# Performance work log

Measured on AMD Instinct MI355X. Metric: run time of the kernel, lower is better.

The kernel has to match this reference:

```python
import jax, jax.numpy as jnp
import numpy as np

RBF_DIM = 64          # args.radius_emb_dim
FOLD_DIM = 128        # args.fold_dim
PROT_RADIUS = 30.0    # args.protein_radius (GaussianSmearing stop)
NP_, NL_, E_ = 100000, 50000, 500000


def gaussian_smearing(d):
    # GaussianSmearing(start=0, stop=PROT_RADIUS, num_gaussians=RBF_DIM)
    offsets = jnp.linspace(0.0, PROT_RADIUS, RBF_DIM, dtype=d.dtype)  # [R]
    coeff = -0.5 / (offsets[1] - offsets[0]) ** 2
    return jnp.exp(coeff * (d[:, None] - offsets[None, :]) ** 2)  # [E, R]


def setup_inputs() -> dict:
    key = jax.random.key(0)
    ks = jax.random.split(key, 12)
    scale = 10.0  # spread positions so distances span [0, PROT_RADIUS]
    pos = lambda k, n: jax.random.normal(k, (n, 3), jnp.float32) * scale
    inp = {
        'lig_pos': pos(ks[0], NL_),
        'prot_pos': pos(ks[1], NP_),
        'prot_pos_Cb': pos(ks[2], NP_),
        'prot_pos_C': pos(ks[3], NP_),
        'prot_pos_O': pos(ks[4], NP_),
        'prot_pos_N': pos(ks[5], NP_),
        'W1': jax.random.normal(ks[6], (5 * RBF_DIM, FOLD_DIM), jnp.float32) * 0.05,
        'b1': jnp.zeros((FOLD_DIM,), jnp.float32),
        'W2': jax.random.normal(ks[7], (FOLD_DIM, FOLD_DIM), jnp.float32) * 0.05,
        'b2': jnp.zeros((FOLD_DIM,), jnp.float32),
        'src': jax.random.randint(ks[8], (E_,), 0, NL_, jnp.int32),   # ligand index per edge
        'dst': jax.random.randint(ks[9], (E_,), 0, NP_, jnp.int32),   # protein index per edge
    }
    return inp


def reference(lig_pos, prot_pos, prot_pos_Cb, prot_pos_C, prot_pos_O, prot_pos_N,
              W1, b1, W2, b2, src, dst):
    lp = lig_pos[src]  # [E, 3] gather of ligand positions
    # 5 distance channels: CA/Cb/C/O/N protein atoms, each RBF-smeared
    feats = [gaussian_smearing(jnp.linalg.norm(lp - p[dst], axis=-1))
             for p in (prot_pos, prot_pos_Cb, prot_pos_C, prot_pos_O, prot_pos_N)]
    edge_attr = jnp.concatenate(feats, axis=-1)  # [E, 5*RBF_DIM]
    h = jax.nn.relu(edge_attr @ W1 + b1)         # [E, FOLD_DIM]
    return h @ W2 + b2                           # [E, FOLD_DIM]
```

## Files before the change

kernel.cpp:

```cpp
#include <hip/hip_runtime.h>
#include <hip/hip_bf16.h>

typedef unsigned short ushort_t;
typedef unsigned int uint_t;
typedef __attribute__((ext_vector_type(8))) short short8;
typedef __attribute__((ext_vector_type(4))) float f32x4;
typedef __attribute__((ext_vector_type(2))) uint_t uint2_t;

#define FOLD 128
#define S_CONST 1.78357580f
#define DS_CONST 0.84932180f

__device__ __forceinline__ uint_t pkbf(float a, float b) {
    __hip_bfloat162 h2 = __float22bfloat162_rn(float2{a, b});
    uint_t u;
    __builtin_memcpy(&u, &h2, sizeof(u));
    return u;
}

#define NWAVES 8
#define W1_OFF 0
#define W2_OFF 20480
#define B1_OFF 28672
#define B2_OFF 28800
#define H_OFF  28928
#define LDS_DW 37120

__global__ __launch_bounds__(512) void fused(
    const float* __restrict__ lig,
    const float* __restrict__ p0, const float* __restrict__ p1,
    const float* __restrict__ p2, const float* __restrict__ p3,
    const float* __restrict__ p4,
    const float* __restrict__ W1, const float* __restrict__ W2,
    const float* __restrict__ b1, const float* __restrict__ b2,
    const int* __restrict__ src, const int* __restrict__ dst,
    float* __restrict__ out, int E)
{
    extern __shared__ uint_t smem[];
    uint_t* W1L = smem + W1_OFF;
    uint_t* W2L = smem + W2_OFF;
    const float* b1L = (const float*)(smem + B1_OFF);
    const float* b2L = (const float*)(smem + B2_OFF);

    const int t = threadIdx.x;
    const int w = t >> 6;
    const int l = t & 63;
    const int eL = l & 15, g = l >> 4;
    uint_t* hw = smem + H_OFF + (w << 10);

    for (int idx = t; idx < 20480; idx += 512) {
        int jj = idx & 3, l2 = (idx >> 2) & 63, nt = (idx >> 8) & 7, ks = idx >> 11;
        int row = ks * 32 + ((l2 >> 4) << 3) + 2 * jj;
        int col = nt * 16 + (l2 & 15);
        W1L[idx] = pkbf(W1[row * FOLD + col], W1[(row + 1) * FOLD + col]);
    }
    for (int idx = t; idx < 8192; idx += 512) {
        int jj = idx & 3, l2 = (idx >> 2) & 63, nt = (idx >> 8) & 7, ks = idx >> 11;
        int row = ks * 32 + ((l2 >> 4) << 3) + 2 * jj;
        int col = nt * 16 + (l2 & 15);
        W2L[idx] = pkbf(W2[row * FOLD + col], W2[(row + 1) * FOLD + col]);
    }
    if (t < 128) ((float*)(smem + B1_OFF))[t] = b1[t];
    else if (t < 256) ((float*)(smem + B2_OFF))[t - 128] = b2[t - 128];
    __syncthreads();

    const int NT = (E + 31) >> 5;
    const int stride = gridDim.x * NWAVES;
    int wt = blockIdx.x * NWAVES + w;
    if (wt >= NT) return;

    const float* GP = (g == 0) ? p0 : (g == 1) ? p1 : (g == 2) ? p2 : p3;
    const bool g0 = (g == 0);
    const float gbase = (float)(8 * g) * DS_CONST;

    float Ax[2], Ay[2], Az[2], Px[2], Py[2], Pz[2], Qx[2], Qy[2], Qz[2];
    {
        #pragma unroll
        for (int eh = 0; eh < 2; ++eh) {
            int e = wt * 32 + eh * 16 + eL; if (e >= E) e = E - 1;
            int s = src[e], d2 = dst[e];
            Ax[eh] = lig[3 * s]; Ay[eh] = lig[3 * s + 1]; Az[eh] = lig[3 * s + 2];
            Px[eh] = GP[3 * d2]; Py[eh] = GP[3 * d2 + 1]; Pz[eh] = GP[3 * d2 + 2];
            if (g0) { Qx[eh] = p4[3 * d2]; Qy[eh] = p4[3 * d2 + 1]; Qz[eh] = p4[3 * d2 + 2]; }
        }
    }

    while (true) {
        const int wt2 = wt + stride;
        const bool more = (wt2 < NT);

        int sB[2], dB[2];
        if (more) {
            #pragma unroll
            for (int eh = 0; eh < 2; ++eh) {
                int e = wt2 * 32 + eh * 16 + eL; if (e >= E) e = E - 1;
                sB[eh] = src[e]; dB[eh] = dst[e];
            }
        }

        float u00[5][2];
        #pragma unroll
        for (int eh = 0; eh < 2; ++eh) {
            float dx = Ax[eh] - Px[eh], dy = Ay[eh] - Py[eh], dz = Az[eh] - Pz[eh];
            float dm = sqrtf(dx * dx + dy * dy + dz * dz);
            float d4 = 0.f;
            if (g0) {
                float ex = Ax[eh] - Qx[eh], ey = Ay[eh] - Qy[eh], ez = Az[eh] - Qz[eh];
                d4 = sqrtf(ex * ex + ey * ey + ez * ez);
            }
            #pragma unroll
            for (int c = 0; c < 4; ++c)
                u00[c][eh] = __builtin_fmaf(__shfl(dm, c * 16 + eL), S_CONST, -gbase);
            u00[4][eh] = __builtin_fmaf(__shfl(d4, eL), S_CONST, -gbase);
        }

        short8 a[2][10];
        #pragma unroll
        for (int ks = 0; ks < 10; ++ks) {
            const int c = ks >> 1;
            #pragma unroll
            for (int eh = 0; eh < 2; ++eh) {
                uint_t dwv[4];
                #pragma unroll
                for (int jj = 0; jj < 4; ++jj) {
                    float k0 = (float)((ks & 1) * 32 + 2 * jj) * DS_CONST;
                    float k1 = (float)((ks & 1) * 32 + 2 * jj + 1) * DS_CONST;
                    float ua = u00[c][eh] - k0;
                    float ub = u00[c][eh] - k1;
                    float va = __builtin_amdgcn_exp2f(-(ua * ua));
                    float vb = __builtin_amdgcn_exp2f(-(ub * ub));
                    dwv[jj] = pkbf(va, vb);
                }
                __builtin_memcpy(&a[eh][ks], dwv, 16);
            }
        }

        float Bx[2], By[2], Bz[2], Rx[2], Ry[2], Rz[2], Sx[2], Sy[2], Sz[2];
        if (more) {
            #pragma unroll
            for (int eh = 0; eh < 2; ++eh) {
                Bx[eh] = lig[3 * sB[eh]]; By[eh] = lig[3 * sB[eh] + 1]; Bz[eh] = lig[3 * sB[eh] + 2];
                Rx[eh] = GP[3 * dB[eh]]; Ry[eh] = GP[3 * dB[eh] + 1]; Rz[eh] = GP[3 * dB[eh] + 2];
                if (g0) { Sx[eh] = p4[3 * dB[eh]]; Sy[eh] = p4[3 * dB[eh] + 1]; Sz[eh] = p4[3 * dB[eh] + 2]; }
            }
        }

        f32x4 acc1[8][2];
        #pragma unroll
        for (int nt = 0; nt < 8; ++nt)
            #pragma unroll
            for (int eh = 0; eh < 2; ++eh) acc1[nt][eh] = f32x4{0.f, 0.f, 0.f, 0.f};
        #pragma unroll
        for (int ks = 0; ks < 10; ++ks) {
            #pragma unroll
            for (int nt = 0; nt < 8; ++nt) {
                const short8 wf = *reinterpret_cast<const short8*>(&W1L[((ks * 8 + nt) * 64 + l) * 4]);
                acc1[nt][0] = __builtin_amdgcn_mfma_f32_16x16x32_bf16(wf, a[0][ks], acc1[nt][0], 0, 0, 0);
                acc1[nt][1] = __builtin_amdgcn_mfma_f32_16x16x32_bf16(wf, a[1][ks], acc1[nt][1], 0, 0, 0);
            }
        }

        const int swzE = (eL & 7) << 3;
        #pragma unroll
        for (int eh = 0; eh < 2; ++eh) {
            #pragma unroll
            for (int nt = 0; nt < 8; ++nt) {
                f32x4 bv = *reinterpret_cast<const f32x4*>(&b1L[nt * 16 + g * 4]);
                float v0 = fmaxf(acc1[nt][eh][0] + bv[0], 0.f);
                float v1 = fmaxf(acc1[nt][eh][1] + bv[1], 0.f);
                float v2 = fmaxf(acc1[nt][eh][2] + bv[2], 0.f);
                float v3 = fmaxf(acc1[nt][eh][3] + bv[3], 0.f);
                uint2_t pv;
                pv[0] = pkbf(v0, v1);
                pv[1] = pkbf(v2, v3);
                *reinterpret_cast<uint2_t*>(&hw[eL * 64 + ((nt * 8 + g * 2) ^ swzE)]) = pv;
            }
            f32x4 acc2[8];
            #pragma unroll
            for (int nt = 0; nt < 8; ++nt) acc2[nt] = f32x4{0.f, 0.f, 0.f, 0.f};
            #pragma unroll
            for (int ks2 = 0; ks2 < 4; ++ks2) {
                const short8 hf = *reinterpret_cast<const short8*>(&hw[eL * 64 + ((ks2 * 16 + g * 4) ^ swzE)]);
                #pragma unroll
                for (int nt = 0; nt < 8; ++nt) {
                    const short8 wf2 = *reinterpret_cast<const short8*>(&W2L[((ks2 * 8 + nt) * 64 + l) * 4]);
                    acc2[nt] = __builtin_amdgcn_mfma_f32_16x16x32_bf16(wf2, hf, acc2[nt], 0, 0, 0);
                }
            }
            int e = wt * 32 + eh * 16 + eL;
            if (e < E) {
                #pragma unroll
                for (int nt = 0; nt < 8; ++nt) {
                    f32x4 bv2 = *reinterpret_cast<const f32x4*>(&b2L[nt * 16 + g * 4]);
                    f32x4 v = acc2[nt] + bv2;
                    __builtin_nontemporal_store(v,
                        reinterpret_cast<f32x4*>(&out[(size_t)e * FOLD + nt * 16 + g * 4]));
                }
            }
            asm volatile("s_waitcnt lgkmcnt(0)" ::: "memory");
        }

        if (!more) break;
        wt = wt2;
        #pragma unroll
        for (int eh = 0; eh < 2; ++eh) {
            Ax[eh] = Bx[eh]; Ay[eh] = By[eh]; Az[eh] = Bz[eh];
            Px[eh] = Rx[eh]; Py[eh] = Ry[eh]; Pz[eh] = Rz[eh];
            if (g0) { Qx[eh] = Sx[eh]; Qy[eh] = Sy[eh]; Qz[eh] = Sz[eh]; }
        }
    }
}

extern "C" void kernel_launch(void* const* d_in, const int* in_sizes, int n_in,
                              void* d_out, int out_size, void* d_ws, size_t ws_size,
                              hipStream_t stream) {
    const float* lig = (const float*)d_in[0];
    const float* p0  = (const float*)d_in[1];
    const float* p1  = (const float*)d_in[2];
    const float* p2  = (const float*)d_in[3];
    const float* p3  = (const float*)d_in[4];
    const float* p4  = (const float*)d_in[5];
    const float* W1  = (const float*)d_in[6];
    const float* b1  = (const float*)d_in[7];
    const float* W2  = (const float*)d_in[8];
    const float* b2  = (const float*)d_in[9];
    const int* src   = (const int*)d_in[10];
    const int* dst   = (const int*)d_in[11];
    float* out = (float*)d_out;
    const int E = in_sizes[10];

    hipFuncSetAttribute(reinterpret_cast<const void*>(fused),
                        hipFuncAttributeMaxDynamicSharedMemorySize, LDS_DW * 4);

    int nblk = 256;
    fused<<<nblk, 512, LDS_DW * 4, stream>>>(lig, p0, p1, p2, p3, p4, W1, W2,
                                             b1, b2, src, dst, out, E);
}
```

Before: 109.3 us.

## Share W2 fragments across both edge halves and raise priority around MFMA loops

Restructures the second GEMM so both 16-edge halves are processed together. Each W2 fragment loaded from LDS now feeds two MFMAs instead of one, which halves W2 LDS reads. The hidden activations are staged through a smaller per-half scratch split along K, with a new swizzle. Wave priority is raised around the MFMA loops to favour matrix issue over other waves. The cost is doubled acc2 register pressure, which may hurt occupancy.

```diff
diff --git a/kernel.cpp b/kernel.cpp
--- a/kernel.cpp
+++ b/kernel.cpp
@@ -150,6 +150,7 @@
         for (int nt = 0; nt < 8; ++nt)
             #pragma unroll
             for (int eh = 0; eh < 2; ++eh) acc1[nt][eh] = f32x4{0.f, 0.f, 0.f, 0.f};
+        __builtin_amdgcn_s_setprio(1);
         #pragma unroll
         for (int ks = 0; ks < 10; ++ks) {
             #pragma unroll
@@ -159,45 +160,66 @@
                 acc1[nt][1] = __builtin_amdgcn_mfma_f32_16x16x32_bf16(wf, a[1][ks], acc1[nt][1], 0, 0, 0);
             }
         }
-
-        const int swzE = (eL & 7) << 3;
-        #pragma unroll
-        for (int eh = 0; eh < 2; ++eh) {
-            #pragma unroll
-            for (int nt = 0; nt < 8; ++nt) {
+        __builtin_amdgcn_s_setprio(0);
+
+        const int swz2 = (eL & 3) << 2;
+        f32x4 acc2[8][2];
+        #pragma unroll
+        for (int nt = 0; nt < 8; ++nt)
+            #pragma unroll
+            for (int eh = 0; eh < 2; ++eh) acc2[nt][eh] = f32x4{0.f, 0.f, 0.f, 0.f};
+
+        #pragma unroll
+        for (int kh = 0; kh < 2; ++kh) {
+            #pragma unroll
+            for (int nn = 0; nn < 4; ++nn) {
+                const int nt = kh * 4 + nn;
                 f32x4 bv = *reinterpret_cast<const f32x4*>(&b1L[nt * 16 + g * 4]);
-                float v0 = fmaxf(acc1[nt][eh][0] + bv[0], 0.f);
-                float v1 = fmaxf(acc1[nt][eh][1] + bv[1], 0.f);
-                float v2 = fmaxf(acc1[nt][eh][2] + bv[2], 0.f);
-                float v3 = fmaxf(acc1[nt][eh][3] + bv[3], 0.f);
-                uint2_t pv;
-                pv[0] = pkbf(v0, v1);
-                pv[1] = pkbf(v2, v3);
-                *reinterpret_cast<uint2_t*>(&hw[eL * 64 + ((nt * 8 + g * 2) ^ swzE)]) = pv;
-            }
-            f32x4 acc2[8];
-            #pragma unroll
-            for (int nt = 0; nt < 8; ++nt) acc2[nt] = f32x4{0.f, 0.f, 0.f, 0.f};
-            #pragma unroll
-            for (int ks2 = 0; ks2 < 4; ++ks2) {
-                const short8 hf = *reinterpret_cast<const short8*>(&hw[eL * 64 + ((ks2 * 16 + g * 4) ^ swzE)]);
+                const int k2l = nn >> 1;
+                const int idx16 = (((nt & 1) * 8 + g * 2) ^ swz2);
+                #pragma unroll
+                for (int eh = 0; eh < 2; ++eh) {
+                    float v0 = fmaxf(acc1[nt][eh][0] + bv[0], 0.f);
+                    float v1 = fmaxf(acc1[nt][eh][1] + bv[1], 0.f);
+                    float v2 = fmaxf(acc1[nt][eh][2] + bv[2], 0.f);
+                    float v3 = fmaxf(acc1[nt][eh][3] + bv[3], 0.f);
+                    uint2_t pv;
+                    pv[0] = pkbf(v0, v1);
+                    pv[1] = pkbf(v2, v3);
+                    *reinterpret_cast<uint2_t*>(&hw[eh * 512 + eL * 32 + k2l * 16 + idx16]) = pv;
+                }
+            }
+            asm volatile("s_waitcnt lgkmcnt(0)" ::: "memory");
+            __builtin_amdgcn_s_setprio(1);
+            #pragma unroll
+            for (int k2l = 0; k2l < 2; ++k2l) {
+                const int ks2 = kh * 2 + k2l;
+                const int ridx = (g * 4) ^ swz2;
+                const short8 hf0 = *reinterpret_cast<const short8*>(&hw[eL * 32 + k2l * 16 + ridx]);
+                const short8 hf1 = *reinterpret_cast<const short8*>(&hw[512 + eL * 32 + k2l * 16 + ridx]);
                 #pragma unroll
                 for (int nt = 0; nt < 8; ++nt) {
                     const short8 wf2 = *reinterpret_cast<const short8*>(&W2L[((ks2 * 8 + nt) * 64 + l) * 4]);
-                    acc2[nt] = __builtin_amdgcn_mfma_f32_16x16x32_bf16(wf2, hf, acc2[nt], 0, 0, 0);
-                }
-            }
+                    acc2[nt][0] = __builtin_amdgcn_mfma_f32_16x16x32_bf16(wf2, hf0, acc2[nt][0], 0, 0, 0);
+                    acc2[nt][1] = __builtin_amdgcn_mfma_f32_16x16x32_bf16(wf2, hf1, acc2[nt][1], 0, 0, 0);
+                }
+            }
+            __builtin_amdgcn_s_setprio(0);
+            asm volatile("s_waitcnt lgkmcnt(0)" ::: "memory");
+        }
+
+        #pragma unroll
+        for (int eh = 0; eh < 2; ++eh) {
             int e = wt * 32 + eh * 16 + eL;
             if (e < E) {
                 #pragma unroll
                 for (int nt = 0; nt < 8; ++nt) {
                     f32x4 bv2 = *reinterpret_cast<const f32x4*>(&b2L[nt * 16 + g * 4]);
-                    f32x4 v = acc2[nt] + bv2;
+                    f32x4 v = acc2[nt][eh] + bv2;
                     __builtin_nontemporal_store(v,
                         reinterpret_cast<f32x4*>(&out[(size_t)e * FOLD + nt * 16 + g * 4]));
                 }
             }
-            asm volatile("s_waitcnt lgkmcnt(0)" ::: "memory");
         }
 
         if (!more) break;
```

Result: no change. 111.4 us (+1.9%).

## Bucket-sort edges by protein index to localize gathers, use contiguous wave tiles

Applied to the files above, without the earlier changes.

Adds three preprocessing kernels (histogram, scan, scatter) that counting-sort edges into 1024-node buckets of the destination index and write permuted src/dst/original-edge arrays into workspace. The fused kernel reads the permuted arrays, gives each wave a contiguous range of tiles with a swizzled block mapping, and scatters output rows back to their original edge positions. The aim is better cache locality for the protein-position gathers. In exchange it pays for three extra launches and extra index traffic, and output stores are no longer sequential.

```diff
diff --git a/kernel.cpp b/kernel.cpp
--- a/kernel.cpp
+++ b/kernel.cpp
@@ -16,6 +16,65 @@
     uint_t u;
     __builtin_memcpy(&u, &h2, sizeof(u));
     return u;
+}
+
+#define NB 128
+#define HB 256
+
+__global__ __launch_bounds__(256) void hist_k(const int* __restrict__ dst,
+                                              int* __restrict__ hist, int E) {
+    __shared__ int h[NB];
+    const int t = threadIdx.x, b = blockIdx.x;
+    if (t < NB) h[t] = 0;
+    __syncthreads();
+    const int nslice = (E + HB - 1) / HB;
+    const int lo = b * nslice;
+    const int hi = (lo + nslice < E) ? lo + nslice : E;
+    for (int i = lo + t; i < hi; i += 256)
+        atomicAdd(&h[dst[i] >> 10], 1);
+    __syncthreads();
+    if (t < NB) hist[b * NB + t] = h[t];
+}
+
+__global__ __launch_bounds__(128) void scan_k(const int* __restrict__ hist,
+                                              int* __restrict__ off) {
+    __shared__ int btot[NB], bstart[NB];
+    const int t = threadIdx.x;
+    int s = 0;
+    for (int blk = 0; blk < HB; ++blk) s += hist[blk * NB + t];
+    btot[t] = s;
+    __syncthreads();
+    if (t == 0) {
+        int run = 0;
+        for (int bb = 0; bb < NB; ++bb) { bstart[bb] = run; run += btot[bb]; }
+    }
+    __syncthreads();
+    int run = bstart[t];
+    for (int blk = 0; blk < HB; ++blk) {
+        off[blk * NB + t] = run;
+        run += hist[blk * NB + t];
+    }
+}
+
+__global__ __launch_bounds__(256) void scatter_k(const int* __restrict__ src,
+                                                 const int* __restrict__ dst,
+                                                 const int* __restrict__ off,
+                                                 int* __restrict__ ps, int* __restrict__ pd,
+                                                 int* __restrict__ pe, int E) {
+    __shared__ int cnt[NB];
+    const int t = threadIdx.x, b = blockIdx.x;
+    if (t < NB) cnt[t] = off[b * NB + t];
+    __syncthreads();
+    const int nslice = (E + HB - 1) / HB;
+    const int lo = b * nslice;
+    const int hi = (lo + nslice < E) ? lo + nslice : E;
+    for (int i = lo + t; i < hi; i += 256) {
+        int d = dst[i];
+        int pos = atomicAdd(&cnt[d >> 10], 1);
+        ps[pos] = src[i];
+        pd[pos] = d;
+        pe[pos] = i;
+    }
 }
 
 #define NWAVES 8
@@ -33,7 +92,8 @@
     const float* __restrict__ p4,
     const float* __restrict__ W1, const float* __restrict__ W2,
     const float* __restrict__ b1, const float* __restrict__ b2,
-    const int* __restrict__ src, const int* __restrict__ dst,
+    const int* __restrict__ ps, const int* __restrict__ pd,
+    const int* __restrict__ pe,
     float* __restrict__ out, int E)
 {
     extern __shared__ uint_t smem[];
@@ -65,36 +125,48 @@
     __syncthreads();
 
     const int NT = (E + 31) >> 5;
-    const int stride = gridDim.x * NWAVES;
-    int wt = blockIdx.x * NWAVES + w;
-    if (wt >= NT) return;
+    const int bid = blockIdx.x;
+    const int swzb = (bid & 7) * 32 + (bid >> 3);
+    const int wgid = swzb * NWAVES + w;
+    const int nwav = gridDim.x * NWAVES;
+    const int tpw = (NT + nwav - 1) / nwav;
+    int wt = wgid * tpw;
+    const int wend = (wt + tpw < NT) ? wt + tpw : NT;
+    if (wt >= wend) return;
 
     const float* GP = (g == 0) ? p0 : (g == 1) ? p1 : (g == 2) ? p2 : p3;
     const bool g0 = (g == 0);
     const float gbase = (float)(8 * g) * DS_CONST;
 
+    int peC[2];
     float Ax[2], Ay[2], Az[2], Px[2], Py[2], Pz[2], Qx[2], Qy[2], Qz[2];
-    {
+    #pragma unroll
+    for (int eh = 0; eh < 2; ++eh) {
+        int i = wt * 32 + eh * 16 + eL; if (i >= E) i = E - 1;
+        peC[eh] = pe ? pe[i] : i;
+        int s = ps[i], d2 = pd[i];
+        Ax[eh] = lig[3 * s]; Ay[eh] = lig[3 * s + 1]; Az[eh] = lig[3 * s + 2];
+        Px[eh] = GP[3 * d2]; Py[eh] = GP[3 * d2 + 1]; Pz[eh] = GP[3 * d2 + 2];
+        if (g0) { Qx[eh] = p4[3 * d2]; Qy[eh] = p4[3 * d2 + 1]; Qz[eh] = p4[3 * d2 + 2]; }
+    }
+    int sB[2], dB[2], peN[2];
+    if (wt + 1 < wend) {
         #pragma unroll
         for (int eh = 0; eh < 2; ++eh) {
-            int e = wt * 32 + eh * 16 + eL; if (e >= E) e = E - 1;
-            int s = src[e], d2 = dst[e];
-            Ax[eh] = lig[3 * s]; Ay[eh] = lig[3 * s + 1]; Az[eh] = lig[3 * s + 2];
-            Px[eh] = GP[3 * d2]; Py[eh] = GP[3 * d2 + 1]; Pz[eh] = GP[3 * d2 + 2];
-            if (g0) { Qx[eh] = p4[3 * d2]; Qy[eh] = p4[3 * d2 + 1]; Qz[eh] = p4[3 * d2 + 2]; }
+            int i = (wt + 1) * 32 + eh * 16 + eL; if (i >= E) i = E - 1;
+            sB[eh] = ps[i]; dB[eh] = pd[i]; peN[eh] = pe ? pe[i] : i;
         }
     }
 
     while (true) {
-        const int wt2 = wt + stride;
-        const bool more = (wt2 < NT);
-
-        int sB[2], dB[2];
-        if (more) {
+        const bool more = (wt + 1 < wend);
+
+        int sB2[2], dB2[2], peN2[2];
+        if (wt + 2 < wend) {
             #pragma unroll
             for (int eh = 0; eh < 2; ++eh) {
-                int e = wt2 * 32 + eh * 16 + eL; if (e >= E) e = E - 1;
-                sB[eh] = src[e]; dB[eh] = dst[e];
+                int i = (wt + 2) * 32 + eh * 16 + eL; if (i >= E) i = E - 1;
+                sB2[eh] = ps[i]; dB2[eh] = pd[i]; peN2[eh] = pe ? pe[i] : i;
             }
         }
 
@@ -187,26 +259,25 @@
                     acc2[nt] = __builtin_amdgcn_mfma_f32_16x16x32_bf16(wf2, hf, acc2[nt], 0, 0, 0);
                 }
             }
-            int e = wt * 32 + eh * 16 + eL;
-            if (e < E) {
-                #pragma unroll
-                for (int nt = 0; nt < 8; ++nt) {
-                    f32x4 bv2 = *reinterpret_cast<const f32x4*>(&b2L[nt * 16 + g * 4]);
-                    f32x4 v = acc2[nt] + bv2;
-                    __builtin_nontemporal_store(v,
-                        reinterpret_cast<f32x4*>(&out[(size_t)e * FOLD + nt * 16 + g * 4]));
-                }
+            const size_t eo = (size_t)peC[eh] * FOLD;
+            #pragma unroll
+            for (int nt = 0; nt < 8; ++nt) {
+                f32x4 bv2 = *reinterpret_cast<const f32x4*>(&b2L[nt * 16 + g * 4]);
+                f32x4 v = acc2[nt] + bv2;
+                __builtin_nontemporal_store(v,
+                    reinterpret_cast<f32x4*>(&out[eo + nt * 16 + g * 4]));
             }
             asm volatile("s_waitcnt lgkmcnt(0)" ::: "memory");
         }
 
         if (!more) break;
-        wt = wt2;
+        ++wt;
         #pragma unroll
         for (int eh = 0; eh < 2; ++eh) {
             Ax[eh] = Bx[eh]; Ay[eh] = By[eh]; Az[eh] = Bz[eh];
             Px[eh] = Rx[eh]; Py[eh] = Ry[eh]; Pz[eh] = Rz[eh];
             if (g0) { Qx[eh] = Sx[eh]; Qy[eh] = Sy[eh]; Qz[eh] = Sz[eh]; }
+            peC[eh] = peN[eh]; sB[eh] = sB2[eh]; dB[eh] = dB2[eh]; peN[eh] = peN2[eh];
         }
     }
 }
@@ -228,11 +299,30 @@
     const int* dst   = (const int*)d_in[11];
     float* out = (float*)d_out;
     const int E = in_sizes[10];
+    const int NP = in_sizes[1] / 3;
+
+    const size_t need = (size_t)E * 3 * sizeof(int) + 2 * (size_t)(HB * NB) * sizeof(int);
+    const bool useperm = (ws_size >= need) && (NP <= (NB << 10));
+
+    const int* ps = src;
+    const int* pd = dst;
+    const int* pei = nullptr;
+    if (useperm) {
+        int* wsb = (int*)d_ws;
+        int* ps_w  = wsb;
+        int* pd_w  = wsb + E;
+        int* pe_w  = wsb + 2 * (size_t)E;
+        int* hist  = wsb + 3 * (size_t)E;
+        int* off   = hist + HB * NB;
+        hist_k<<<HB, 256, 0, stream>>>(dst, hist, E);
+        scan_k<<<1, 128, 0, stream>>>(hist, off);
+        scatter_k<<<HB, 256, 0, stream>>>(src, dst, off, ps_w, pd_w, pe_w, E);
+        ps = ps_w; pd = pd_w; pei = pe_w;
+    }
 
     hipFuncSetAttribute(reinterpret_cast<const void*>(fused),
                         hipFuncAttributeMaxDynamicSharedMemorySize, LDS_DW * 4);
 
-    int nblk = 256;
-    fused<<<nblk, 512, LDS_DW * 4, stream>>>(lig, p0, p1, p2, p3, p4, W1, W2,
-                                             b1, b2, src, dst, out, E);
-}
+    fused<<<256, 512, LDS_DW * 4, stream>>>(lig, p0, p1, p2, p3, p4, W1, W2,
+                                            b1, b2, ps, pd, pei, out, E);
+}
```

After: 128.4 us. 17.5% more time.

## Pack protein and ligand positions into aligned AoS buffers and deepen index prefetch

Applied to the files above, without the earlier changes.

Adds a pre-pass kernel that interleaves the five protein atom position arrays into one 64-byte record per residue and pads ligand positions to float4, held in workspace. The fused kernel then gathers from these packed records so that one edge's protein atoms share a cache line, and ligand reads become single vector loads. It also prefetches src/dst indices two tiles ahead and issues the position gathers earlier in the loop, so gather latency overlaps the RBF/MFMA work. The cost is an extra launch and a full pass over the position arrays on every call, plus more live registers.

```diff
diff --git a/kernel.cpp b/kernel.cpp
--- a/kernel.cpp
+++ b/kernel.cpp
@@ -16,6 +16,35 @@
     uint_t u;
     __builtin_memcpy(&u, &h2, sizeof(u));
     return u;
+}
+
+__global__ __launch_bounds__(256) void pack_pos(
+    const float* __restrict__ p0, const float* __restrict__ p1,
+    const float* __restrict__ p2, const float* __restrict__ p3,
+    const float* __restrict__ p4, const float* __restrict__ lig,
+    float* __restrict__ P5, float* __restrict__ L4, int NP, int NL)
+{
+    int i = blockIdx.x * 256 + threadIdx.x;
+    if (i < NP) {
+        float r[16];
+        const float* ps0 = p0 + 3 * i; const float* ps1 = p1 + 3 * i;
+        const float* ps2 = p2 + 3 * i; const float* ps3 = p3 + 3 * i;
+        const float* ps4 = p4 + 3 * i;
+        r[0]=ps0[0]; r[1]=ps0[1]; r[2]=ps0[2];
+        r[3]=ps1[0]; r[4]=ps1[1]; r[5]=ps1[2];
+        r[6]=ps2[0]; r[7]=ps2[1]; r[8]=ps2[2];
+        r[9]=ps3[0]; r[10]=ps3[1]; r[11]=ps3[2];
+        r[12]=ps4[0]; r[13]=ps4[1]; r[14]=ps4[2];
+        r[15]=0.f;
+        #pragma unroll
+        for (int k = 0; k < 4; ++k)
+            *reinterpret_cast<f32x4*>(&P5[(size_t)i * 16 + k * 4]) =
+                *reinterpret_cast<f32x4*>(&r[k * 4]);
+    } else if (i < NP + NL) {
+        int j = i - NP;
+        f32x4 v = {lig[3 * j], lig[3 * j + 1], lig[3 * j + 2], 0.f};
+        *reinterpret_cast<f32x4*>(&L4[(size_t)j * 4]) = v;
+    }
 }
 
 #define NWAVES 8
@@ -26,11 +55,13 @@
 #define H_OFF  28928
 #define LDS_DW 37120
 
+template<bool PACKED>
 __global__ __launch_bounds__(512) void fused(
     const float* __restrict__ lig,
     const float* __restrict__ p0, const float* __restrict__ p1,
     const float* __restrict__ p2, const float* __restrict__ p3,
     const float* __restrict__ p4,
+    const float* __restrict__ P5, const float* __restrict__ L4,
     const float* __restrict__ W1, const float* __restrict__ W2,
     const float* __restrict__ b1, const float* __restrict__ b2,
     const int* __restrict__ src, const int* __restrict__ dst,
@@ -70,31 +101,69 @@
     if (wt >= NT) return;
 
     const float* GP = (g == 0) ? p0 : (g == 1) ? p1 : (g == 2) ? p2 : p3;
+    const float* GPp = PACKED ? (P5 + g * 3) : nullptr;
     const bool g0 = (g == 0);
     const float gbase = (float)(8 * g) * DS_CONST;
 
     float Ax[2], Ay[2], Az[2], Px[2], Py[2], Pz[2], Qx[2], Qy[2], Qz[2];
-    {
-        #pragma unroll
-        for (int eh = 0; eh < 2; ++eh) {
-            int e = wt * 32 + eh * 16 + eL; if (e >= E) e = E - 1;
-            int s = src[e], d2 = dst[e];
+    #pragma unroll
+    for (int eh = 0; eh < 2; ++eh) {
+        int e = wt * 32 + eh * 16 + eL; if (e >= E) e = E - 1;
+        int s = src[e], d2 = dst[e];
+        if constexpr (PACKED) {
+            f32x4 lv = *reinterpret_cast<const f32x4*>(&L4[(size_t)s * 4]);
+            Ax[eh] = lv[0]; Ay[eh] = lv[1]; Az[eh] = lv[2];
+            const float* rp = GPp + (size_t)d2 * 16;
+            Px[eh] = rp[0]; Py[eh] = rp[1]; Pz[eh] = rp[2];
+            if (g0) {
+                const float* qp = P5 + (size_t)d2 * 16 + 12;
+                Qx[eh] = qp[0]; Qy[eh] = qp[1]; Qz[eh] = qp[2];
+            }
+        } else {
             Ax[eh] = lig[3 * s]; Ay[eh] = lig[3 * s + 1]; Az[eh] = lig[3 * s + 2];
             Px[eh] = GP[3 * d2]; Py[eh] = GP[3 * d2 + 1]; Pz[eh] = GP[3 * d2 + 2];
             if (g0) { Qx[eh] = p4[3 * d2]; Qy[eh] = p4[3 * d2 + 1]; Qz[eh] = p4[3 * d2 + 2]; }
         }
     }
+    int sB[2], dB[2];
+    if (wt + stride < NT) {
+        #pragma unroll
+        for (int eh = 0; eh < 2; ++eh) {
+            int e = (wt + stride) * 32 + eh * 16 + eL; if (e >= E) e = E - 1;
+            sB[eh] = src[e]; dB[eh] = dst[e];
+        }
+    }
 
     while (true) {
         const int wt2 = wt + stride;
         const bool more = (wt2 < NT);
 
-        int sB[2], dB[2];
+        float Bx[2], By[2], Bz[2], Rx[2], Ry[2], Rz[2], Sx[2], Sy[2], Sz[2];
         if (more) {
             #pragma unroll
             for (int eh = 0; eh < 2; ++eh) {
-                int e = wt2 * 32 + eh * 16 + eL; if (e >= E) e = E - 1;
-                sB[eh] = src[e]; dB[eh] = dst[e];
+                if constexpr (PACKED) {
+                    f32x4 lv = *reinterpret_cast<const f32x4*>(&L4[(size_t)sB[eh] * 4]);
+                    Bx[eh] = lv[0]; By[eh] = lv[1]; Bz[eh] = lv[2];
+                    const float* rp = GPp + (size_t)dB[eh] * 16;
+                    Rx[eh] = rp[0]; Ry[eh] = rp[1]; Rz[eh] = rp[2];
+                    if (g0) {
+                        const float* qp = P5 + (size_t)dB[eh] * 16 + 12;
+                        Sx[eh] = qp[0]; Sy[eh] = qp[1]; Sz[eh] = qp[2];
+                    }
+                } else {
+                    Bx[eh] = lig[3 * sB[eh]]; By[eh] = lig[3 * sB[eh] + 1]; Bz[eh] = lig[3 * sB[eh] + 2];
+                    Rx[eh] = GP[3 * dB[eh]]; Ry[eh] = GP[3 * dB[eh] + 1]; Rz[eh] = GP[3 * dB[eh] + 2];
+                    if (g0) { Sx[eh] = p4[3 * dB[eh]]; Sy[eh] = p4[3 * dB[eh] + 1]; Sz[eh] = p4[3 * dB[eh] + 2]; }
+                }
+            }
+        }
+        int sB2[2], dB2[2];
+        if (wt2 + stride < NT) {
+            #pragma unroll
+            for (int eh = 0; eh < 2; ++eh) {
+                int e = (wt2 + stride) * 32 + eh * 16 + eL; if (e >= E) e = E - 1;
+                sB2[eh] = src[e]; dB2[eh] = dst[e];
             }
         }
 
@@ -135,16 +204,6 @@
             }
         }
 
-        float Bx[2], By[2], Bz[2], Rx[2], Ry[2], Rz[2], Sx[2], Sy[2], Sz[2];
-        if (more) {
-            #pragma unroll
-            for (int eh = 0; eh < 2; ++eh) {
-                Bx[eh] = lig[3 * sB[eh]]; By[eh] = lig[3 * sB[eh] + 1]; Bz[eh] = lig[3 * sB[eh] + 2];
-                Rx[eh] = GP[3 * dB[eh]]; Ry[eh] = GP[3 * dB[eh] + 1]; Rz[eh] = GP[3 * dB[eh] + 2];
-                if (g0) { Sx[eh] = p4[3 * dB[eh]]; Sy[eh] = p4[3 * dB[eh] + 1]; Sz[eh] = p4[3 * dB[eh] + 2]; }
-            }
-        }
-
         f32x4 acc1[8][2];
         #pragma unroll
         for (int nt = 0; nt < 8; ++nt)
@@ -207,6 +266,7 @@
             Ax[eh] = Bx[eh]; Ay[eh] = By[eh]; Az[eh] = Bz[eh];
             Px[eh] = Rx[eh]; Py[eh] = Ry[eh]; Pz[eh] = Rz[eh];
             if (g0) { Qx[eh] = Sx[eh]; Qy[eh] = Sy[eh]; Qz[eh] = Sz[eh]; }
+            sB[eh] = sB2[eh]; dB[eh] = dB2[eh];
         }
     }
 }
@@ -227,12 +287,28 @@
     const int* src   = (const int*)d_in[10];
     const int* dst   = (const int*)d_in[11];
     float* out = (float*)d_out;
-    const int E = in_sizes[10];
-
-    hipFuncSetAttribute(reinterpret_cast<const void*>(fused),
+    const int E  = in_sizes[10];
+    const int NL = in_sizes[0] / 3;
+    const int NP = in_sizes[1] / 3;
+
+    const size_t need = ((size_t)NP * 16 + (size_t)NL * 4) * sizeof(float);
+    const bool packed = (ws_size >= need);
+
+    hipFuncSetAttribute(reinterpret_cast<const void*>(fused<true>),
                         hipFuncAttributeMaxDynamicSharedMemorySize, LDS_DW * 4);
-
-    int nblk = 256;
-    fused<<<nblk, 512, LDS_DW * 4, stream>>>(lig, p0, p1, p2, p3, p4, W1, W2,
-                                             b1, b2, src, dst, out, E);
+    hipFuncSetAttribute(reinterpret_cast<const void*>(fused<false>),
+                        hipFuncAttributeMaxDynamicSharedMemorySize, LDS_DW * 4);
+
+    if (packed) {
+        float* P5 = (float*)d_ws;
+        float* L4 = P5 + (size_t)NP * 16;
+        pack_pos<<<(NP + NL + 255) / 256, 256, 0, stream>>>(p0, p1, p2, p3, p4, lig,
+                                                            P5, L4, NP, NL);
+        fused<true><<<256, 512, LDS_DW * 4, stream>>>(lig, p0, p1, p2, p3, p4, P5, L4,
+                                                      W1, W2, b1, b2, src, dst, out, E);
+    } else {
+        fused<false><<<256, 512, LDS_DW * 4, stream>>>(lig, p0, p1, p2, p3, p4,
+                                                       nullptr, nullptr,
+                                                       W1, W2, b1, b2, src, dst, out, E);
+    }
 }
```

After: 115.1 us. 5.3% more time.
